# Optimization experiments

Measured on AMD Instinct MI355X. Metric: run time of the kernel, lower is better.

## Reference

```python
import jax, jax.numpy as jnp
import numpy as np

N, M, B, L, D = 100000, 256, 8, 128, 64
COORD_MAX = 1024


def setup_inputs() -> dict:
    key = jax.random.key(0)
    ks = jax.random.split(key, 9)
    # batch ids sorted so the original loop's centroid_offset == column index
    clu_b = jnp.sort(jax.random.randint(ks[0], (N, 1), 0, B))
    cen_b = jnp.sort(jax.random.randint(ks[1], (M, 1), 0, B))
    clu_xyz = jax.random.randint(ks[2], (N, 3), 0, COORD_MAX)
    cen_xyz = jax.random.randint(ks[3], (M, 3), 0, COORD_MAX)
    return {
        "cluster_coords": jnp.concatenate([clu_b, clu_xyz], axis=1).astype(jnp.int32),
        "centroid_coords": jnp.concatenate([cen_b, cen_xyz], axis=1).astype(jnp.int32),
        "cluster_feats": jax.random.normal(ks[4], (N, L), jnp.float32),
        "centroid_feats": jax.random.normal(ks[5], (M, L), jnp.float32),
        "centroid_conf": jax.random.uniform(ks[6], (M, 1), jnp.float32),
        "W": jax.random.normal(ks[7], (L, D), jnp.float32) * 0.05,
        "b": jax.random.normal(ks[8], (D,), jnp.float32) * 0.05,
    }


def reference(cluster_coords, centroid_coords, cluster_feats, centroid_feats,
              centroid_conf, W, b):
    # pointwise Conv3d(k=1) == linear on features
    clu = cluster_feats @ W + b                      # [N, D]
    nrm = jnp.maximum(jnp.linalg.norm(clu, axis=1, keepdims=True), 1e-12)
    clu = clu / nrm                                  # F.normalize(p=2, dim=1)
    cen = centroid_conf * (centroid_feats @ W + b)   # [M, D]

    # same-batch mask replaces the python loop + scatter
    valid = cluster_coords[:, 0][:, None] == centroid_coords[:, 0][None, :]  # [N, M]

    # pairwise L2 distance on spatial coords via squared expansion (exact for small ints)
    cc = cluster_coords[:, 1:].astype(jnp.float32)   # [N, 3]
    ec = centroid_coords[:, 1:].astype(jnp.float32)  # [M, 3]
    d2 = (jnp.sum(cc * cc, axis=1)[:, None]
          + jnp.sum(ec * ec, axis=1)[None, :]
          - 2.0 * cc @ ec.T)
    dist = jnp.maximum(jnp.sqrt(jnp.maximum(d2, 0.0)), 0.1)  # clamp(min=0.1)

    logits = jnp.where(valid, -dist, -jnp.inf)
    attn = jax.nn.softmax(logits, axis=-1)           # per-row over same-batch centroids
    attn = jnp.where(valid, attn, 0.0)               # rows w/ no centroids -> 0 (matches zeros init)

    out = (clu @ cen.T) * attn                       # [N, M]
    return out
```

## Files before the change

kernel.cpp:

```cpp
#include <hip/hip_runtime.h>
#include <stdint.h>


#define NN 100000
#define MM 256
#define LL 128
#define DD 64
#define NTILES (NN / 16)

typedef float f32x4 __attribute__((ext_vector_type(4)));
typedef __bf16 bf16x8 __attribute__((ext_vector_type(8)));

union U16x8 { uint4 u; bf16x8 v; unsigned short s[8]; };

static __device__ __forceinline__ unsigned short f2bf(float f) {
  union { float f; unsigned int i; } t; t.f = f;
  unsigned int x = t.i;
  x += 0x7fffu + ((x >> 16) & 1u);
  return (unsigned short)(x >> 16);
}

__global__ __launch_bounds__(256) void prep_kernel(
    const int* __restrict__ cen_coords,
    const float* __restrict__ cen_feats,
    const float* __restrict__ conf,
    const float* __restrict__ W,
    const float* __restrict__ bvec,
    unsigned short* __restrict__ cen_ws,
    unsigned short* __restrict__ wt_ws,
    float4* __restrict__ cmeta_ws)
{
  int tid = threadIdx.x;
  if (blockIdx.x < 16) {
    int m = blockIdx.x * 16 + (tid >> 4);
    int c = tid & 15;
    float a0 = 0.f, a1 = 0.f, a2 = 0.f, a3 = 0.f;
    for (int l = 0; l < LL; l++) {
      float f = cen_feats[m * LL + l];
      const float* wr = W + l * DD + c;
      a0 += f * wr[0];  a1 += f * wr[16];
      a2 += f * wr[32]; a3 += f * wr[48];
    }
    float cf = conf[m];
    cen_ws[m * DD + c +  0] = f2bf(cf * (a0 + bvec[c +  0]));
    cen_ws[m * DD + c + 16] = f2bf(cf * (a1 + bvec[c + 16]));
    cen_ws[m * DD + c + 32] = f2bf(cf * (a2 + bvec[c + 32]));
    cen_ws[m * DD + c + 48] = f2bf(cf * (a3 + bvec[c + 48]));
  } else {
    for (int i = tid; i < LL * DD; i += 256) {
      int l = i >> 6, d = i & 63;
      wt_ws[d * LL + l] = f2bf(W[l * DD + d]);
    }
    {
      int4 cc = ((const int4*)cen_coords)[tid];
      float4 f; f.x = (float)cc.x; f.y = (float)cc.y; f.z = (float)cc.z; f.w = (float)cc.w;
      cmeta_ws[tid] = f;
    }
  }
}

__global__ __launch_bounds__(256) void main_kernel(
    const int4* __restrict__ clu_coords4,
    const float* __restrict__ feats,
    const float* __restrict__ bvec,
    const unsigned short* __restrict__ cen_ws,
    const unsigned short* __restrict__ wt_ws,
    const float4* __restrict__ cmeta,
    float* __restrict__ out)
{
  __shared__ __align__(16) unsigned short clu_s[4][16 * 72];

  int tid = threadIdx.x;
  int wave = tid >> 6, lane = tid & 63;
  int q = lane >> 4, c = lane & 15;
  int tile = blockIdx.x * 4 + wave;
  bool live = tile < NTILES;

  float inv_nrm[4];
  if (live) {
    f32x4 acc[4] = {{0,0,0,0},{0,0,0,0},{0,0,0,0},{0,0,0,0}};
    const float4* fb = (const float4*)(feats + (size_t)(tile * 16 + c) * LL);
    const uint4* wb = (const uint4*)wt_ws;
#pragma unroll
    for (int ks = 0; ks < 4; ks++) {
      float4 f0 = fb[ks * 8 + q * 2];
      float4 f1 = fb[ks * 8 + q * 2 + 1];
      U16x8 a;
      a.s[0] = f2bf(f0.x); a.s[1] = f2bf(f0.y); a.s[2] = f2bf(f0.z); a.s[3] = f2bf(f0.w);
      a.s[4] = f2bf(f1.x); a.s[5] = f2bf(f1.y); a.s[6] = f2bf(f1.z); a.s[7] = f2bf(f1.w);
#pragma unroll
      for (int nt = 0; nt < 4; nt++) {
        U16x8 b; b.u = wb[(nt * 16 + c) * 16 + ks * 4 + q];
        acc[nt] = __builtin_amdgcn_mfma_f32_16x16x32_bf16(a.v, b.v, acc[nt], 0, 0, 0);
      }
    }
#pragma unroll
    for (int nt = 0; nt < 4; nt++) {
      float bv = bvec[nt * 16 + c];
      acc[nt][0] += bv; acc[nt][1] += bv; acc[nt][2] += bv; acc[nt][3] += bv;
    }
#pragma unroll
    for (int r = 0; r < 4; r++) {
      float s = acc[0][r]*acc[0][r] + acc[1][r]*acc[1][r] + acc[2][r]*acc[2][r] + acc[3][r]*acc[3][r];
      s += __shfl_xor(s, 1); s += __shfl_xor(s, 2); s += __shfl_xor(s, 4); s += __shfl_xor(s, 8);
      inv_nrm[r] = 1.0f / fmaxf(sqrtf(s), 1e-12f);
    }
#pragma unroll
    for (int nt = 0; nt < 4; nt++)
#pragma unroll
      for (int r = 0; r < 4; r++)
        clu_s[wave][(q * 4 + r) * 72 + nt * 16 + c] = f2bf(acc[nt][r]);
  }
  __syncthreads();
  if (!live) return;

  int rb[4]; float rx[4], ry[4], rz[4];
#pragma unroll
  for (int r = 0; r < 4; r++) {
    int4 rm = clu_coords4[tile * 16 + q * 4 + r];
    rb[r] = rm.x; rx[r] = (float)rm.y; ry[r] = (float)rm.z; rz[r] = (float)rm.w;
  }

  float dv[16][4];
  float dmin[4] = {1e30f, 1e30f, 1e30f, 1e30f};
#pragma unroll
  for (int mt = 0; mt < 16; mt++) {
    float4 cm = cmeta[mt * 16 + c];
    int cbatch = (int)cm.x;
#pragma unroll
    for (int r = 0; r < 4; r++) {
      float dx = rx[r] - cm.y, dy = ry[r] - cm.z, dz = rz[r] - cm.w;
      float d = fmaxf(sqrtf(dx*dx + dy*dy + dz*dz), 0.1f);
      d = (cbatch == rb[r]) ? d : 1e30f;
      dv[mt][r] = d;
      dmin[r] = fminf(dmin[r], d);
    }
  }
#pragma unroll
  for (int r = 0; r < 4; r++) {
    dmin[r] = fminf(dmin[r], __shfl_xor(dmin[r], 1));
    dmin[r] = fminf(dmin[r], __shfl_xor(dmin[r], 2));
    dmin[r] = fminf(dmin[r], __shfl_xor(dmin[r], 4));
    dmin[r] = fminf(dmin[r], __shfl_xor(dmin[r], 8));
    dmin[r] = fminf(dmin[r], 1e29f);
  }
  float rsum[4] = {0.f, 0.f, 0.f, 0.f};
#pragma unroll
  for (int mt = 0; mt < 16; mt++)
#pragma unroll
    for (int r = 0; r < 4; r++) {
      float e = __expf(fminf(dmin[r] - dv[mt][r], 0.f));
      dv[mt][r] = e;
      rsum[r] += e;
    }
  float scale[4];
#pragma unroll
  for (int r = 0; r < 4; r++) {
    rsum[r] += __shfl_xor(rsum[r], 1);
    rsum[r] += __shfl_xor(rsum[r], 2);
    rsum[r] += __shfl_xor(rsum[r], 4);
    rsum[r] += __shfl_xor(rsum[r], 8);
    scale[r] = (rsum[r] > 0.f) ? inv_nrm[r] / rsum[r] : 0.f;
  }

  const uint4* cb = (const uint4*)(clu_s[wave]);
  U16x8 a0, a1;
  a0.u = cb[c * 9 + q];
  a1.u = cb[c * 9 + 4 + q];

  const uint4* cenb = (const uint4*)cen_ws;
  size_t orow = (size_t)(tile * 16) * MM;
#pragma unroll
  for (int mt = 0; mt < 16; mt++) {
    U16x8 b0, b1;
    b0.u = cenb[(mt * 16 + c) * 8 + q];
    b1.u = cenb[(mt * 16 + c) * 8 + 4 + q];
    f32x4 dacc = {0, 0, 0, 0};
    dacc = __builtin_amdgcn_mfma_f32_16x16x32_bf16(a0.v, b0.v, dacc, 0, 0, 0);
    dacc = __builtin_amdgcn_mfma_f32_16x16x32_bf16(a1.v, b1.v, dacc, 0, 0, 0);
    int m = mt * 16 + c;
#pragma unroll
    for (int r = 0; r < 4; r++)
      out[orow + (size_t)(q * 4 + r) * MM + m] = dacc[r] * dv[mt][r] * scale[r];
  }
}

extern "C" void kernel_launch(void* const* d_in, const int* in_sizes, int n_in,
                              void* d_out, int out_size, void* d_ws, size_t ws_size,
                              hipStream_t stream) {
  const int* clu_coords = (const int*)d_in[0];
  const int* cen_coords = (const int*)d_in[1];
  const float* clu_feats = (const float*)d_in[2];
  const float* cen_feats = (const float*)d_in[3];
  const float* conf      = (const float*)d_in[4];
  const float* W         = (const float*)d_in[5];
  const float* bvec      = (const float*)d_in[6];
  float* out = (float*)d_out;

  char* ws = (char*)d_ws;
  unsigned short* cen_ws = (unsigned short*)ws;
  unsigned short* wt_ws  = (unsigned short*)(ws + 32768);
  float4* cmeta_ws       = (float4*)(ws + 32768 + 16384);

  prep_kernel<<<17, 256, 0, stream>>>(cen_coords, cen_feats, conf, W, bvec,
                                      cen_ws, wt_ws, cmeta_ws);
  main_kernel<<<(NTILES + 3) / 4, 256, 0, stream>>>(
      (const int4*)clu_coords, clu_feats, bvec, cen_ws, wt_ws, cmeta_ws, out);
}
```

Before: 198.4 us.

## Encode batch into x-coordinate and recompute distances instead of storing them

```diff
diff --git a/kernel.cpp b/kernel.cpp
--- a/kernel.cpp
+++ b/kernel.cpp
@@ -53,7 +53,11 @@
     }
     {
       int4 cc = ((const int4*)cen_coords)[tid];
-      float4 f; f.x = (float)cc.x; f.y = (float)cc.y; f.z = (float)cc.z; f.w = (float)cc.w;
+      float4 f;
+      f.x = (float)cc.y + 4096.0f * (float)cc.x;
+      f.y = (float)cc.z;
+      f.z = (float)cc.w;
+      f.w = 0.0f;
       cmeta_ws[tid] = f;
     }
   }
@@ -74,11 +78,10 @@
   int wave = tid >> 6, lane = tid & 63;
   int q = lane >> 4, c = lane & 15;
   int tile = blockIdx.x * 4 + wave;
-  bool live = tile < NTILES;
-
-  float inv_nrm[4];
-  if (live) {
-    f32x4 acc[4] = {{0,0,0,0},{0,0,0,0},{0,0,0,0},{0,0,0,0}};
+  if (tile >= NTILES) return;
+
+  f32x4 acc[4] = {{0,0,0,0},{0,0,0,0},{0,0,0,0},{0,0,0,0}};
+  {
     const float4* fb = (const float4*)(feats + (size_t)(tile * 16 + c) * LL);
     const uint4* wb = (const uint4*)wt_ws;
 #pragma unroll
@@ -94,65 +97,73 @@
         acc[nt] = __builtin_amdgcn_mfma_f32_16x16x32_bf16(a.v, b.v, acc[nt], 0, 0, 0);
       }
     }
-#pragma unroll
-    for (int nt = 0; nt < 4; nt++) {
-      float bv = bvec[nt * 16 + c];
-      acc[nt][0] += bv; acc[nt][1] += bv; acc[nt][2] += bv; acc[nt][3] += bv;
-    }
-#pragma unroll
-    for (int r = 0; r < 4; r++) {
-      float s = acc[0][r]*acc[0][r] + acc[1][r]*acc[1][r] + acc[2][r]*acc[2][r] + acc[3][r]*acc[3][r];
-      s += __shfl_xor(s, 1); s += __shfl_xor(s, 2); s += __shfl_xor(s, 4); s += __shfl_xor(s, 8);
-      inv_nrm[r] = 1.0f / fmaxf(sqrtf(s), 1e-12f);
-    }
-#pragma unroll
-    for (int nt = 0; nt < 4; nt++)
-#pragma unroll
-      for (int r = 0; r < 4; r++)
-        clu_s[wave][(q * 4 + r) * 72 + nt * 16 + c] = f2bf(acc[nt][r]);
-  }
-  __syncthreads();
-  if (!live) return;
-
-  int rb[4]; float rx[4], ry[4], rz[4];
+  }
+#pragma unroll
+  for (int nt = 0; nt < 4; nt++) {
+    float bv = bvec[nt * 16 + c];
+    acc[nt][0] += bv; acc[nt][1] += bv; acc[nt][2] += bv; acc[nt][3] += bv;
+  }
+  float inv_nrm[4];
+#pragma unroll
+  for (int r = 0; r < 4; r++) {
+    float s = acc[0][r]*acc[0][r] + acc[1][r]*acc[1][r] + acc[2][r]*acc[2][r] + acc[3][r]*acc[3][r];
+    s += __shfl_xor(s, 1); s += __shfl_xor(s, 2); s += __shfl_xor(s, 4); s += __shfl_xor(s, 8);
+    inv_nrm[r] = 1.0f / fmaxf(sqrtf(s), 1e-12f);
+  }
+#pragma unroll
+  for (int nt = 0; nt < 4; nt++)
+#pragma unroll
+    for (int r = 0; r < 4; r++)
+      clu_s[wave][(q * 4 + r) * 72 + nt * 16 + c] = f2bf(acc[nt][r]);
+
+  __builtin_amdgcn_sched_barrier(0);
+
+  const uint4* cb = (const uint4*)(clu_s[wave]);
+  U16x8 a0, a1;
+  a0.u = cb[c * 9 + q];
+  a1.u = cb[c * 9 + 4 + q];
+
+  float rx[4], ry[4], rz[4];
 #pragma unroll
   for (int r = 0; r < 4; r++) {
     int4 rm = clu_coords4[tile * 16 + q * 4 + r];
-    rb[r] = rm.x; rx[r] = (float)rm.y; ry[r] = (float)rm.z; rz[r] = (float)rm.w;
-  }
-
-  float dv[16][4];
-  float dmin[4] = {1e30f, 1e30f, 1e30f, 1e30f};
+    rx[r] = (float)rm.y + 4096.0f * (float)rm.x;
+    ry[r] = (float)rm.z;
+    rz[r] = (float)rm.w;
+  }
+
+  float d2m[4] = {1e30f, 1e30f, 1e30f, 1e30f};
 #pragma unroll
   for (int mt = 0; mt < 16; mt++) {
     float4 cm = cmeta[mt * 16 + c];
-    int cbatch = (int)cm.x;
 #pragma unroll
     for (int r = 0; r < 4; r++) {
-      float dx = rx[r] - cm.y, dy = ry[r] - cm.z, dz = rz[r] - cm.w;
-      float d = fmaxf(sqrtf(dx*dx + dy*dy + dz*dz), 0.1f);
-      d = (cbatch == rb[r]) ? d : 1e30f;
-      dv[mt][r] = d;
-      dmin[r] = fminf(dmin[r], d);
-    }
-  }
-#pragma unroll
-  for (int r = 0; r < 4; r++) {
-    dmin[r] = fminf(dmin[r], __shfl_xor(dmin[r], 1));
-    dmin[r] = fminf(dmin[r], __shfl_xor(dmin[r], 2));
-    dmin[r] = fminf(dmin[r], __shfl_xor(dmin[r], 4));
-    dmin[r] = fminf(dmin[r], __shfl_xor(dmin[r], 8));
-    dmin[r] = fminf(dmin[r], 1e29f);
-  }
+      float dx = rx[r] - cm.x, dy = ry[r] - cm.y, dz = rz[r] - cm.z;
+      float d2 = dx * dx + dy * dy + dz * dz;
+      d2m[r] = fminf(d2m[r], d2);
+    }
+  }
+  float dmv[4];
+#pragma unroll
+  for (int r = 0; r < 4; r++) {
+    d2m[r] = fminf(d2m[r], __shfl_xor(d2m[r], 1));
+    d2m[r] = fminf(d2m[r], __shfl_xor(d2m[r], 2));
+    d2m[r] = fminf(d2m[r], __shfl_xor(d2m[r], 4));
+    d2m[r] = fminf(d2m[r], __shfl_xor(d2m[r], 8));
+    dmv[r] = fmaxf(sqrtf(d2m[r]), 0.1f);
+  }
+
   float rsum[4] = {0.f, 0.f, 0.f, 0.f};
 #pragma unroll
-  for (int mt = 0; mt < 16; mt++)
+  for (int mt = 0; mt < 16; mt++) {
+    float4 cm = cmeta[mt * 16 + c];
 #pragma unroll
     for (int r = 0; r < 4; r++) {
-      float e = __expf(fminf(dmin[r] - dv[mt][r], 0.f));
-      dv[mt][r] = e;
-      rsum[r] += e;
-    }
+      float dx = rx[r] - cm.x, dy = ry[r] - cm.y, dz = rz[r] - cm.z;
+      float d = fmaxf(sqrtf(dx * dx + dy * dy + dz * dz), 0.1f);
+      rsum[r] += __expf(dmv[r] - d);
+    }
+  }
   float scale[4];
 #pragma unroll
   for (int r = 0; r < 4; r++) {
@@ -160,16 +171,15 @@
     rsum[r] += __shfl_xor(rsum[r], 2);
     rsum[r] += __shfl_xor(rsum[r], 4);
     rsum[r] += __shfl_xor(rsum[r], 8);
-    scale[r] = (rsum[r] > 0.f) ? inv_nrm[r] / rsum[r] : 0.f;
-  }
-
-  const uint4* cb = (const uint4*)(clu_s[wave]);
-  U16x8 a0, a1;
-  a0.u = cb[c * 9 + q];
-  a1.u = cb[c * 9 + 4 + q];
+    scale[r] = (d2m[r] < 4.0e6f) ? inv_nrm[r] / rsum[r] : 0.f;
+  }
 
   const uint4* cenb = (const uint4*)cen_ws;
-  size_t orow = (size_t)(tile * 16) * MM;
+  float* op[4];
+#pragma unroll
+  for (int r = 0; r < 4; r++)
+    op[r] = out + (size_t)(tile * 16 + q * 4 + r) * MM + c;
+
 #pragma unroll
   for (int mt = 0; mt < 16; mt++) {
     U16x8 b0, b1;
@@ -178,10 +188,14 @@
     f32x4 dacc = {0, 0, 0, 0};
     dacc = __builtin_amdgcn_mfma_f32_16x16x32_bf16(a0.v, b0.v, dacc, 0, 0, 0);
     dacc = __builtin_amdgcn_mfma_f32_16x16x32_bf16(a1.v, b1.v, dacc, 0, 0, 0);
-    int m = mt * 16 + c;
-#pragma unroll
-    for (int r = 0; r < 4; r++)
-      out[orow + (size_t)(q * 4 + r) * MM + m] = dacc[r] * dv[mt][r] * scale[r];
+    float4 cm = cmeta[mt * 16 + c];
+#pragma unroll
+    for (int r = 0; r < 4; r++) {
+      float dx = rx[r] - cm.x, dy = ry[r] - cm.y, dz = rz[r] - cm.z;
+      float d = fmaxf(sqrtf(dx * dx + dy * dy + dz * dz), 0.1f);
+      float e = __expf(dmv[r] - d);
+      op[r][mt * 16] = dacc[r] * (e * scale[r]);
+    }
   }
 }
 
```

Result: slower. 203.9 us (+2.7%).
